# Performance work log

Measured on AMD Instinct MI355X. Metric: run time of the kernel, lower is better.

Reference implementation:

```python
import jax, jax.numpy as jnp
import numpy as np

N = 100000   # nodes
E = 600000   # edges (before self loops)
D = 128      # dim_latent = H*F
H = 4        # heads
F = 32       # out_feats per head
L = 3        # num GATConv layers (conv_0 + 2)


def setup_inputs() -> dict:
    key = jax.random.key(0)
    ks = jax.random.split(key, 10)
    return {
        "weights": jax.random.normal(ks[0], (N,), jnp.float32),
        "lin_W": jax.random.normal(ks[1], (D, 1), jnp.float32) * 0.1,
        "lin_b": jnp.zeros((D,), jnp.float32),
        "fc_W": jax.random.normal(ks[2], (L, D, D), jnp.float32) * (1.0 / np.sqrt(D)),
        "attn_l": jax.random.normal(ks[3], (L, H, F), jnp.float32) * 0.1,
        "attn_r": jax.random.normal(ks[4], (L, H, F), jnp.float32) * 0.1,
        "conv_b": jnp.zeros((L, D), jnp.float32),
        "pred_W": jax.random.normal(ks[5], (1, D), jnp.float32) * 0.1,
        "pred_b": jnp.zeros((1,), jnp.float32),
        "src": jax.random.randint(ks[6], (E,), 0, N, jnp.int32),
        "dst": jax.random.randint(ks[7], (E,), 0, N, jnp.int32),
    }


def _leaky(x, slope):
    return jnp.where(x >= 0, x, slope * x)


def _gat_conv(x, fc_W, attn_l, attn_r, bias, src, dst):
    # DGL GATConv: bias-free fc, per-head additive attention, edge softmax over dst
    h = (x @ fc_W.T).reshape(N, H, F)                      # [N,H,F]
    el = jnp.sum(h * attn_l[None], axis=-1)                # [N,H]
    er = jnp.sum(h * attn_r[None], axis=-1)                # [N,H]
    e = _leaky(el[src] + er[dst], 0.2)                     # [Etot,H]
    m = jax.ops.segment_max(e, dst, num_segments=N)        # [N,H]
    a = jnp.exp(e - m[dst])                                # [Etot,H]
    s = jax.ops.segment_sum(a, dst, num_segments=N)        # [N,H]
    alpha = a / s[dst]                                     # [Etot,H]
    msg = h[src] * alpha[:, :, None]                       # [Etot,H,F]
    out = jax.ops.segment_sum(msg, dst, num_segments=N)    # [N,H,F]
    out = out + bias.reshape(H, F)[None]
    return out.reshape(N, H * F)


def reference(weights, lin_W, lin_b, fc_W, attn_l, attn_r, conv_b, pred_W, pred_b, src, dst):
    # add self loops (dgl.add_self_loop)
    loop = jnp.arange(N, dtype=src.dtype)
    s_full = jnp.concatenate([src, loop])
    d_full = jnp.concatenate([dst, loop])

    x = weights[:, None] @ lin_W.T + lin_b                 # [N,D]
    for i in range(L):
        if i > 0:
            x = _leaky(x, 0.01)                            # nn.LeakyReLU default
        x = _gat_conv(x, fc_W[i], attn_l[i], attn_r[i], conv_b[i], s_full, d_full)
    logits = x @ pred_W.T + pred_b                         # [N,1]
    return logits
```

## Files before the change

kernel.cpp:

```cpp
#include <hip/hip_runtime.h>
#include <hip/hip_bf16.h>
#include <math.h>


__device__ __forceinline__ float leaky02(float x) {
    return x >= 0.f ? x : 0.2f * x;
}
__device__ __forceinline__ float leaky01(float x) {
    return x >= 0.f ? x : 0.01f * x;
}

__device__ __forceinline__ unsigned short f2bf(float f) {
    unsigned u = __float_as_uint(f);
    unsigned r = u + 0x7FFFu + ((u >> 16) & 1u);
    return (unsigned short)(r >> 16);
}
__device__ __forceinline__ float bf2f(unsigned short s) {
    return __uint_as_float(((unsigned)s) << 16);
}

typedef __attribute__((ext_vector_type(8))) short bf16x8;
typedef __attribute__((ext_vector_type(8))) unsigned short u16x8;
typedef __attribute__((ext_vector_type(4))) float f32x4;

__global__ __launch_bounds__(1024) void prep_kernel(
    int* __restrict__ deg, int N,
    const float* __restrict__ fc_W, const float* __restrict__ attn_l,
    const float* __restrict__ attn_r,
    short* __restrict__ Wh, short* __restrict__ Wl,
    short* __restrict__ Mh, short* __restrict__ Ml,
    const float* __restrict__ lW, const float* __restrict__ lb,
    const float* __restrict__ cb2, const float* __restrict__ pW,
    const float* __restrict__ pb,
    float* __restrict__ c1, float* __restrict__ c2, float* __restrict__ prm)
{
    const int nbi = (N + 1023) >> 10;
    const int b = blockIdx.x;
    const int t = threadIdx.x;

    if (b < nbi) {
        int i = b * 1024 + t;
        if (i < N) deg[i] = 1;
        if (i < 2 * 16384) {
            const float* W = fc_W + 16384;
            int l    = i >> 14;
            int p    = i & 16383;
            int j    = p & 7;
            int lane = (p >> 3) & 63;
            int c    = (p >> 9) & 7;
            int kk   = p >> 12;
            int mr   = lane & 15;
            int quad = lane >> 4;
            int row  = c * 16 + mr;
            int d    = kk * 32 + quad * 8 + j;
            float f = W[(size_t)l * 16384 + row * 128 + d];
            unsigned short hi = f2bf(f);
            Wh[i] = (short)hi;
            Wl[i] = (short)f2bf(f - bf2f(hi));
        }
    } else if (b < nbi + 2) {
        int l = b - nbi;
        const float* W  = fc_W + (size_t)(l + 1) * 16384;
        const float* al = attn_l + (l + 1) * 128;
        const float* ar = attn_r + (l + 1) * 128;
        short* mh = Mh + (size_t)l * 16 * 128;
        short* ml = Ml + (size_t)l * 16 * 128;
        int r = t >> 7;
        int d = t & 127;
        int hh = r & 3;
        const float* av = (r < 4) ? al : ar;
        float s = 0.f;
#pragma unroll
        for (int f = 0; f < 32; ++f)
            s += W[(size_t)(hh * 32 + f) * 128 + d] * av[hh * 32 + f];
        unsigned short hi = f2bf(s);
        mh[r * 128 + d] = (short)hi;
        ml[r * 128 + d] = (short)f2bf(s - bf2f(hi));
        mh[(r + 8) * 128 + d] = 0;
        ml[(r + 8) * 128 + d] = 0;
    } else {
        __shared__ float sh1[128], sh2[128], sh3[128], sh4[128], sh5[128];
        const float* W0 = fc_W;
        const float* al = attn_l;
        const float* ar = attn_r;
        int j = t >> 3, sub = t & 7;
        float s1 = 0.f, s2 = 0.f;
        int d0 = sub * 16;
#pragma unroll
        for (int k = 0; k < 16; ++k) {
            float wv = W0[j * 128 + d0 + k];
            s1 += lW[d0 + k] * wv;
            s2 += lb[d0 + k] * wv;
        }
#pragma unroll
        for (int m = 1; m <= 4; m <<= 1) {
            s1 += __shfl_xor(s1, m, 64);
            s2 += __shfl_xor(s2, m, 64);
        }
        if (sub == 0) {
            c1[j] = s1; c2[j] = s2;
            sh1[j] = s1 * al[j]; sh2[j] = s2 * al[j];
            sh3[j] = s1 * ar[j]; sh4[j] = s2 * ar[j];
            sh5[j] = cb2[j] * pW[j];
        }
        __syncthreads();
        if (t < 4) {
            float p = 0.f, q = 0.f, r = 0.f, s = 0.f;
            for (int f = 0; f < 32; ++f) {
                p += sh1[t * 32 + f]; q += sh2[t * 32 + f];
                r += sh3[t * 32 + f]; s += sh4[t * 32 + f];
            }
            prm[t] = p; prm[4 + t] = q; prm[8 + t] = r; prm[12 + t] = s;
        }
        if (t == 0) {
            float cs = 0.f;
            for (int k = 0; k < 128; ++k) cs += sh5[k];
            prm[16] = cs + pb[0];
        }
    }
}

__global__ __launch_bounds__(256) void deg_count_slot_kernel(
    const int* __restrict__ dst, int* __restrict__ deg,
    int* __restrict__ slot, int E)
{
    int i = blockIdx.x * 256 + threadIdx.x;
    if (i < E) slot[i] = atomicAdd(&deg[dst[i]], 1);
}

#define SCAN_TILE 1024

__global__ __launch_bounds__(256) void scanA_kernel(
    const int* __restrict__ deg, int* __restrict__ bsum, int N)
{
    __shared__ int ws[4];
    int b = blockIdx.x, t = threadIdx.x;
    int base = b * SCAN_TILE + t * 4;
    int s = 0;
#pragma unroll
    for (int k = 0; k < 4; ++k) {
        int i = base + k;
        if (i < N) s += deg[i];
    }
#pragma unroll
    for (int m = 32; m >= 1; m >>= 1) s += __shfl_xor(s, m, 64);
    if ((t & 63) == 0) ws[t >> 6] = s;
    __syncthreads();
    if (t == 0) bsum[b] = ws[0] + ws[1] + ws[2] + ws[3];
}

__global__ __launch_bounds__(1024) void scanB_kernel(
    int* __restrict__ bsum, int* __restrict__ bpre, int* __restrict__ rowp,
    int NB, int N)
{
    __shared__ int sh[1024];
    int t = threadIdx.x;
    int v = (t < NB) ? bsum[t] : 0;
    sh[t] = v;
    __syncthreads();
    for (int off = 1; off < 1024; off <<= 1) {
        int u = (t >= off) ? sh[t - off] : 0;
        __syncthreads();
        sh[t] += u;
        __syncthreads();
    }
    if (t < NB) bpre[t] = sh[t] - v;
    if (t == 1023) rowp[N] = sh[1023];
}

__global__ __launch_bounds__(256) void scanC_kernel(
    const int* __restrict__ deg, const int* __restrict__ bpre,
    int* __restrict__ rowp, int* __restrict__ col, int N)
{
    __shared__ int sh[256];
    int b = blockIdx.x, t = threadIdx.x;
    int base = b * SCAN_TILE + t * 4;
    int v[4];
#pragma unroll
    for (int k = 0; k < 4; ++k) {
        int i = base + k;
        v[k] = (i < N) ? deg[i] : 0;
    }
    int tsum = v[0] + v[1] + v[2] + v[3];
    sh[t] = tsum;
    __syncthreads();
    for (int off = 1; off < 256; off <<= 1) {
        int u = (t >= off) ? sh[t - off] : 0;
        __syncthreads();
        sh[t] += u;
        __syncthreads();
    }
    int pre = bpre[b] + sh[t] - tsum;
#pragma unroll
    for (int k = 0; k < 4; ++k) {
        int i = base + k;
        if (i < N) {
            rowp[i] = pre;
            col[pre] = i;
        }
        pre += v[k];
    }
}

__global__ __launch_bounds__(256) void scatter2_kernel(
    const int* __restrict__ src, const int* __restrict__ dst,
    const int* __restrict__ slot, const int* __restrict__ rowp,
    int* __restrict__ col, int E)
{
    int i = blockIdx.x * 256 + threadIdx.x;
    if (i < E) col[rowp[dst[i]] + slot[i]] = src[i];
}

__global__ __launch_bounds__(256) void agg0_kernel(
    const float* __restrict__ w, const float* __restrict__ c1,
    const float* __restrict__ c2, const float* __restrict__ prm,
    const int* __restrict__ rowp, const int* __restrict__ col,
    const float* __restrict__ bias, unsigned short* __restrict__ xout, int N)
{
    const int lane = threadIdx.x & 63;
    const int q    = lane >> 4;
    const int l16  = lane & 15;
    const int v    = blockIdx.x * 16 + (threadIdx.x >> 6) * 4 + q;
    if (v >= N) return;

    const int r0 = rowp[v], r1 = rowp[v + 1];
    const int head = l16 >> 2;
    const int e4   = l16 & 3;
    const int f0   = l16 * 8;
    const float pl = prm[head],     ql = prm[4 + head];
    const float pr = prm[8 + head], qr = prm[12 + head];

    const float wv  = w[v];
    const float erq = wv * pr + qr;
    const float mref = leaky02(wv * pl + ql + erq);

    float S = 0.f, Sw = 0.f;
    for (int j = r0 + e4; j < r1; j += 4) {
        int u = col[j];
        float wu = w[u];
        float e = leaky02(wu * pl + ql + erq);
        float d = fminf(e - mref, 80.f);
        float p = __expf(d);
        S += p; Sw += p * wu;
    }
    S  += __shfl_xor(S, 1, 64);  S  += __shfl_xor(S, 2, 64);
    Sw += __shfl_xor(Sw, 1, 64); Sw += __shfl_xor(Sw, 2, 64);
    const float t = Sw / S;

    float4 a0 = *reinterpret_cast<const float4*>(&c1[f0]);
    float4 a1 = *reinterpret_cast<const float4*>(&c1[f0 + 4]);
    float4 g0 = *reinterpret_cast<const float4*>(&c2[f0]);
    float4 g1 = *reinterpret_cast<const float4*>(&c2[f0 + 4]);
    float4 b0 = *reinterpret_cast<const float4*>(&bias[f0]);
    float4 b1 = *reinterpret_cast<const float4*>(&bias[f0 + 4]);
    const float aa[8] = {a0.x, a0.y, a0.z, a0.w, a1.x, a1.y, a1.z, a1.w};
    const float gg[8] = {g0.x, g0.y, g0.z, g0.w, g1.x, g1.y, g1.z, g1.w};
    const float bb[8] = {b0.x, b0.y, b0.z, b0.w, b1.x, b1.y, b1.z, b1.w};

    u16x8 o;
#pragma unroll
    for (int k = 0; k < 8; ++k)
        o[k] = f2bf(leaky01(t * aa[k] + gg[k] + bb[k]));
    *reinterpret_cast<u16x8*>(&xout[(size_t)v * 128 + f0]) = o;
}

__global__ __launch_bounds__(256) void gemm_mfma_kernel(
    const unsigned short* __restrict__ xb, const short* __restrict__ Wh,
    const short* __restrict__ Wl, const short* __restrict__ Mh,
    const short* __restrict__ Ml, unsigned short* __restrict__ hb,
    float* __restrict__ el, float* __restrict__ er,
    const float* __restrict__ pW, float* __restrict__ yel,
    int N, int mode)
{
    const int lane = threadIdx.x & 63;
    const int wv   = threadIdx.x >> 6;
    const int m0   = blockIdx.x * 128 + wv * 32;
    const int mr   = lane & 15;
    const int quad = lane >> 4;

    int r0 = m0 + mr;      if (r0 > N - 1) r0 = N - 1;
    int r1 = m0 + 16 + mr; if (r1 > N - 1) r1 = N - 1;
    const unsigned short* xp0 = xb + (size_t)r0 * 128 + quad * 8;
    const unsigned short* xp1 = xb + (size_t)r1 * 128 + quad * 8;

    f32x4 acc0[8], acc1[8], acce0, acce1;
#pragma unroll
    for (int c = 0; c < 8; ++c) {
        acc0[c] = (f32x4){0.f, 0.f, 0.f, 0.f};
        acc1[c] = (f32x4){0.f, 0.f, 0.f, 0.f};
    }
    acce0 = (f32x4){0.f, 0.f, 0.f, 0.f};
    acce1 = (f32x4){0.f, 0.f, 0.f, 0.f};

#pragma unroll
    for (int kk = 0; kk < 4; ++kk) {
        bf16x8 a0 = *reinterpret_cast<const bf16x8*>(xp0 + kk * 32);
        bf16x8 a1 = *reinterpret_cast<const bf16x8*>(xp1 + kk * 32);

        const int kb = kk * 32 + quad * 8;
        bf16x8 bh[8], bl[8];
#pragma unroll
        for (int c = 0; c < 8; ++c) {
            const size_t wo = (size_t)((kk * 8 + c) * 64 + lane) * 8;
            bh[c] = *reinterpret_cast<const bf16x8*>(Wh + wo);
            bl[c] = *reinterpret_cast<const bf16x8*>(Wl + wo);
        }
        bf16x8 eh = *reinterpret_cast<const bf16x8*>(Mh + (size_t)mr * 128 + kb);
        bf16x8 eo = *reinterpret_cast<const bf16x8*>(Ml + (size_t)mr * 128 + kb);
#pragma unroll
        for (int c = 0; c < 8; ++c) {
            acc0[c] = __builtin_amdgcn_mfma_f32_16x16x32_bf16(a0, bh[c], acc0[c], 0, 0, 0);
            acc0[c] = __builtin_amdgcn_mfma_f32_16x16x32_bf16(a0, bl[c], acc0[c], 0, 0, 0);
            acc1[c] = __builtin_amdgcn_mfma_f32_16x16x32_bf16(a1, bh[c], acc1[c], 0, 0, 0);
            acc1[c] = __builtin_amdgcn_mfma_f32_16x16x32_bf16(a1, bl[c], acc1[c], 0, 0, 0);
        }
        acce0 = __builtin_amdgcn_mfma_f32_16x16x32_bf16(a0, eh, acce0, 0, 0, 0);
        acce0 = __builtin_amdgcn_mfma_f32_16x16x32_bf16(a0, eo, acce0, 0, 0, 0);
        acce1 = __builtin_amdgcn_mfma_f32_16x16x32_bf16(a1, eh, acce1, 0, 0, 0);
        acce1 = __builtin_amdgcn_mfma_f32_16x16x32_bf16(a1, eo, acce1, 0, 0, 0);
    }

    if (mode == 0) {
#pragma unroll
        for (int i = 0; i < 4; ++i) {
            int rowA = m0 + quad * 4 + i;
            if (rowA < N) {
                unsigned short* hp = hb + (size_t)rowA * 128 + mr;
#pragma unroll
                for (int c = 0; c < 8; ++c) hp[c * 16] = f2bf(acc0[c][i]);
                if (mr < 4)       el[(size_t)rowA * 4 + mr]       = acce0[i];
                else if (mr < 8)  er[(size_t)rowA * 4 + (mr - 4)] = acce0[i];
            }
            int rowB = m0 + 16 + quad * 4 + i;
            if (rowB < N) {
                unsigned short* hp = hb + (size_t)rowB * 128 + mr;
#pragma unroll
                for (int c = 0; c < 8; ++c) hp[c * 16] = f2bf(acc1[c][i]);
                if (mr < 4)       el[(size_t)rowB * 4 + mr]       = acce1[i];
                else if (mr < 8)  er[(size_t)rowB * 4 + (mr - 4)] = acce1[i];
            }
        }
    } else {
        float pw[8];
#pragma unroll
        for (int c = 0; c < 8; ++c) pw[c] = pW[mr + c * 16];
#pragma unroll
        for (int i = 0; i < 4; ++i) {
            int rowA = m0 + quad * 4 + i;
            {
                float y[4];
#pragma unroll
                for (int h = 0; h < 4; ++h)
                    y[h] = acc0[2 * h][i] * pw[2 * h] + acc0[2 * h + 1][i] * pw[2 * h + 1];
#pragma unroll
                for (int d = 1; d < 16; d <<= 1) {
#pragma unroll
                    for (int h = 0; h < 4; ++h) y[h] += __shfl_xor(y[h], d, 64);
                }
                if (rowA < N) {
                    if (mr < 4) {
                        float2 o; o.x = y[mr]; o.y = acce0[i];
                        *reinterpret_cast<float2*>(&yel[(size_t)rowA * 8 + mr * 2]) = o;
                    } else if (mr < 8) {
                        er[(size_t)rowA * 4 + (mr - 4)] = acce0[i];
                    }
                }
            }
            int rowB = m0 + 16 + quad * 4 + i;
            {
                float y[4];
#pragma unroll
                for (int h = 0; h < 4; ++h)
                    y[h] = acc1[2 * h][i] * pw[2 * h] + acc1[2 * h + 1][i] * pw[2 * h + 1];
#pragma unroll
                for (int d = 1; d < 16; d <<= 1) {
#pragma unroll
                    for (int h = 0; h < 4; ++h) y[h] += __shfl_xor(y[h], d, 64);
                }
                if (rowB < N) {
                    if (mr < 4) {
                        float2 o; o.x = y[mr]; o.y = acce1[i];
                        *reinterpret_cast<float2*>(&yel[(size_t)rowB * 8 + mr * 2]) = o;
                    } else if (mr < 8) {
                        er[(size_t)rowB * 4 + (mr - 4)] = acce1[i];
                    }
                }
            }
        }
    }
}

__global__ __launch_bounds__(256) void agg_mid_kernel(
    const unsigned short* __restrict__ hb, const float* __restrict__ el,
    const float* __restrict__ er, const int* __restrict__ rowp,
    const int* __restrict__ col, const float* __restrict__ bias,
    unsigned short* __restrict__ xout, int N)
{
    const int lane = threadIdx.x & 63;
    const int q    = lane >> 4;
    const int l16  = lane & 15;
    const int v    = blockIdx.x * 16 + (threadIdx.x >> 6) * 4 + q;
    if (v >= N) return;

    const int r0 = rowp[v], r1 = rowp[v + 1];
    const int head = l16 >> 2;
    const int f0   = l16 * 8;
    const float erq = er[(size_t)v * 4 + head];
    const float el_self = el[(size_t)v * 4 + head];
    const float mref = leaky02(el_self + erq);

    float s = 0.f;
    float acc[8];
#pragma unroll
    for (int k = 0; k < 8; ++k) acc[k] = 0.f;

    float elA = el_self;
    u16x8 hvA = *reinterpret_cast<const u16x8*>(&hb[(size_t)v * 128 + f0]);
    int jB = (r0 + 1 < r1) ? r0 + 1 : r1 - 1;
    int uB = col[jB];
    float elB = el[(size_t)uB * 4 + head];
    u16x8 hvB = *reinterpret_cast<const u16x8*>(&hb[(size_t)uB * 128 + f0]);

    for (int j = r0; j < r1; j += 2) {
        int jA2 = (j + 2 < r1) ? j + 2 : r1 - 1;
        int uA2 = col[jA2];
        float elA2 = el[(size_t)uA2 * 4 + head];
        u16x8 hvA2 = *reinterpret_cast<const u16x8*>(&hb[(size_t)uA2 * 128 + f0]);

        {
            float e = leaky02(elA + erq);
            float d = fminf(e - mref, 80.f);
            float p = __expf(d);
            s += p;
#pragma unroll
            for (int k = 0; k < 8; ++k) acc[k] += p * bf2f(hvA[k]);
        }

        if (j + 1 < r1) {
            int jB2 = (j + 3 < r1) ? j + 3 : r1 - 1;
            int uB2 = col[jB2];
            float elB2 = el[(size_t)uB2 * 4 + head];
            u16x8 hvB2 = *reinterpret_cast<const u16x8*>(&hb[(size_t)uB2 * 128 + f0]);

            float e = leaky02(elB + erq);
            float d = fminf(e - mref, 80.f);
            float p = __expf(d);
            s += p;
#pragma unroll
            for (int k = 0; k < 8; ++k) acc[k] += p * bf2f(hvB[k]);

            elB = elB2; hvB = hvB2;
        }
        elA = elA2; hvA = hvA2;
    }
    const float is = 1.f / s;

    float4 b0 = *reinterpret_cast<const float4*>(&bias[f0]);
    float4 b1 = *reinterpret_cast<const float4*>(&bias[f0 + 4]);
    const float bb[8] = {b0.x, b0.y, b0.z, b0.w, b1.x, b1.y, b1.z, b1.w};

    u16x8 o;
#pragma unroll
    for (int k = 0; k < 8; ++k) o[k] = f2bf(leaky01(acc[k] * is + bb[k]));
    *reinterpret_cast<u16x8*>(&xout[(size_t)v * 128 + f0]) = o;
}

__global__ __launch_bounds__(256) void agg2_kernel(
    const float* __restrict__ yel, const float* __restrict__ er,
    const int* __restrict__ rowp, const int* __restrict__ col,
    const float* __restrict__ prm, float* __restrict__ logits, int N)
{
    const int lane = threadIdx.x & 63;
    const int q    = lane >> 4;
    const int l16  = lane & 15;
    const int v    = blockIdx.x * 16 + (threadIdx.x >> 6) * 4 + q;
    if (v >= N) return;

    const int r0 = rowp[v], r1 = rowp[v + 1];
    const int head = l16 >> 2;
    const int e4   = l16 & 3;
    const float erq = er[(size_t)v * 4 + head];

    float2 selfy = *reinterpret_cast<const float2*>(&yel[(size_t)v * 8 + head * 2]);
    const float mref = leaky02(selfy.y + erq);

    float S = 0.f, A = 0.f;
    for (int j = r0 + e4; j < r1; j += 4) {
        int u = col[j];
        float2 c = *reinterpret_cast<const float2*>(&yel[(size_t)u * 8 + head * 2]);
        float e = leaky02(c.y + erq);
        float d = fminf(e - mref, 80.f);
        float p = __expf(d);
        S += p; A += p * c.x;
    }
    S += __shfl_xor(S, 1, 64); S += __shfl_xor(S, 2, 64);
    A += __shfl_xor(A, 1, 64); A += __shfl_xor(A, 2, 64);
    float part = A / S;
    part += __shfl_xor(part, 4, 64);
    part += __shfl_xor(part, 8, 64);
    if (l16 == 0) logits[v] = part + prm[16];
}

extern "C" void kernel_launch(void* const* d_in, const int* in_sizes, int n_in,
                              void* d_out, int out_size, void* d_ws, size_t ws_size,
                              hipStream_t stream)
{
    const float* weights = (const float*)d_in[0];
    const float* lin_W   = (const float*)d_in[1];
    const float* lin_b   = (const float*)d_in[2];
    const float* fc_W    = (const float*)d_in[3];
    const float* attn_l  = (const float*)d_in[4];
    const float* attn_r  = (const float*)d_in[5];
    const float* conv_b  = (const float*)d_in[6];
    const float* pred_W  = (const float*)d_in[7];
    const float* pred_b  = (const float*)d_in[8];
    const int*   src     = (const int*)d_in[9];
    const int*   dst     = (const int*)d_in[10];

    const int N = in_sizes[0];
    const int E = in_sizes[9];
    const int NB = (N + SCAN_TILE - 1) / SCAN_TILE;
    const int NBI = (N + 1023) / 1024;

    unsigned short* xb = (unsigned short*)d_ws;
    unsigned short* hb = xb + (size_t)N * 128;
    float* el  = (float*)(hb + (size_t)N * 128);
    float* er  = el + (size_t)N * 4;
    float* yel = er + (size_t)N * 4;
    float* c1  = yel + (size_t)N * 8;
    float* c2  = c1 + 128;
    float* prm = c2 + 128;
    short* Whs = (short*)(prm + 32);
    short* Wls = Whs + 2 * 16384;
    short* Mhs = Wls + 2 * 16384;
    short* Mls = Mhs + 2 * 2048;
    int*   deg  = (int*)(Mls + 2 * 2048);
    int*   rowp = deg + N;
    int*   slot = rowp + (N + 1);
    int*   col  = slot + E;
    int*   bsum = col + (E + N);
    int*   bpre = bsum + NB;

    prep_kernel<<<NBI + 3, 1024, 0, stream>>>(
        deg, N, fc_W, attn_l, attn_r, Whs, Wls, Mhs, Mls,
        lin_W, lin_b, conv_b + 2 * 128, pred_W, pred_b, c1, c2, prm);

    deg_count_slot_kernel<<<(E + 255) / 256, 256, 0, stream>>>(dst, deg, slot, E);
    scanA_kernel<<<NB, 256, 0, stream>>>(deg, bsum, N);
    scanB_kernel<<<1, 1024, 0, stream>>>(bsum, bpre, rowp, NB, N);
    scanC_kernel<<<NB, 256, 0, stream>>>(deg, bpre, rowp, col, N);
    scatter2_kernel<<<(E + 255) / 256, 256, 0, stream>>>(src, dst, slot, rowp, col, E);

    agg0_kernel<<<(N + 15) / 16, 256, 0, stream>>>(
        weights, c1, c2, prm, rowp, col, conv_b, xb, N);

    gemm_mfma_kernel<<<(N + 127) / 128, 256, 0, stream>>>(
        xb, Whs, Wls, Mhs, Mls, hb, el, er, pred_W, yel, N, 0);
    agg_mid_kernel<<<(N + 15) / 16, 256, 0, stream>>>(
        hb, el, er, rowp, col, conv_b + 128, xb, N);

    gemm_mfma_kernel<<<(N + 127) / 128, 256, 0, stream>>>(
        xb, Whs + 16384, Wls + 16384, Mhs + 2048, Mls + 2048,
        hb, el, er, pred_W, yel, N, 1);
    agg2_kernel<<<(N + 15) / 16, 256, 0, stream>>>(
        yel, er, rowp, col, prm, (float*)d_out, N);
}
```

Baseline: 251.8 us.

## Replace three-pass prefix scan with single-pass atomic-base block scan

Merges the three scan kernels into one kernel. Each 1024-node block scans its degrees locally and claims a global base offset through an atomicAdd on a counter zeroed in prep_kernel. Because blocks claim bases in arbitrary order, rows are no longer globally ordered, so the aggregation kernels now compute row ends as rowp[v]+deg[v] instead of reading rowp[v+1]. This removes two kernel launches and their serial dependencies, at the cost of an extra deg read per node and a non-monotonic CSR layout.

```diff
diff --git a/kernel.cpp b/kernel.cpp
--- a/kernel.cpp
+++ b/kernel.cpp
@@ -32,11 +32,13 @@
     const float* __restrict__ lW, const float* __restrict__ lb,
     const float* __restrict__ cb2, const float* __restrict__ pW,
     const float* __restrict__ pb,
-    float* __restrict__ c1, float* __restrict__ c2, float* __restrict__ prm)
+    float* __restrict__ c1, float* __restrict__ c2, float* __restrict__ prm,
+    int* __restrict__ base_ctr)
 {
     const int nbi = (N + 1023) >> 10;
     const int b = blockIdx.x;
     const int t = threadIdx.x;
+    if (b == 0 && t == 0) *base_ctr = 0;
 
     if (b < nbi) {
         int i = b * 1024 + t;
@@ -128,34 +130,15 @@
     if (i < E) slot[i] = atomicAdd(&deg[dst[i]], 1);
 }
 
-#define SCAN_TILE 1024
-
-__global__ __launch_bounds__(256) void scanA_kernel(
-    const int* __restrict__ deg, int* __restrict__ bsum, int N)
-{
-    __shared__ int ws[4];
+__global__ __launch_bounds__(1024) void scan_kernel(
+    const int* __restrict__ deg, int* __restrict__ base_ctr,
+    int* __restrict__ rowp, int* __restrict__ col, int N)
+{
+    __shared__ int sh[1024];
+    __shared__ int sbase;
     int b = blockIdx.x, t = threadIdx.x;
-    int base = b * SCAN_TILE + t * 4;
-    int s = 0;
-#pragma unroll
-    for (int k = 0; k < 4; ++k) {
-        int i = base + k;
-        if (i < N) s += deg[i];
-    }
-#pragma unroll
-    for (int m = 32; m >= 1; m >>= 1) s += __shfl_xor(s, m, 64);
-    if ((t & 63) == 0) ws[t >> 6] = s;
-    __syncthreads();
-    if (t == 0) bsum[b] = ws[0] + ws[1] + ws[2] + ws[3];
-}
-
-__global__ __launch_bounds__(1024) void scanB_kernel(
-    int* __restrict__ bsum, int* __restrict__ bpre, int* __restrict__ rowp,
-    int NB, int N)
-{
-    __shared__ int sh[1024];
-    int t = threadIdx.x;
-    int v = (t < NB) ? bsum[t] : 0;
+    int i = b * 1024 + t;
+    int v = (i < N) ? deg[i] : 0;
     sh[t] = v;
     __syncthreads();
     for (int off = 1; off < 1024; off <<= 1) {
@@ -164,41 +147,12 @@
         sh[t] += u;
         __syncthreads();
     }
-    if (t < NB) bpre[t] = sh[t] - v;
-    if (t == 1023) rowp[N] = sh[1023];
-}
-
-__global__ __launch_bounds__(256) void scanC_kernel(
-    const int* __restrict__ deg, const int* __restrict__ bpre,
-    int* __restrict__ rowp, int* __restrict__ col, int N)
-{
-    __shared__ int sh[256];
-    int b = blockIdx.x, t = threadIdx.x;
-    int base = b * SCAN_TILE + t * 4;
-    int v[4];
-#pragma unroll
-    for (int k = 0; k < 4; ++k) {
-        int i = base + k;
-        v[k] = (i < N) ? deg[i] : 0;
-    }
-    int tsum = v[0] + v[1] + v[2] + v[3];
-    sh[t] = tsum;
+    if (t == 1023) sbase = atomicAdd(base_ctr, sh[1023]);
     __syncthreads();
-    for (int off = 1; off < 256; off <<= 1) {
-        int u = (t >= off) ? sh[t - off] : 0;
-        __syncthreads();
-        sh[t] += u;
-        __syncthreads();
-    }
-    int pre = bpre[b] + sh[t] - tsum;
-#pragma unroll
-    for (int k = 0; k < 4; ++k) {
-        int i = base + k;
-        if (i < N) {
-            rowp[i] = pre;
-            col[pre] = i;
-        }
-        pre += v[k];
+    int pre = sbase + sh[t] - v;
+    if (i < N) {
+        rowp[i] = pre;
+        col[pre] = i;
     }
 }
 
@@ -214,8 +168,9 @@
 __global__ __launch_bounds__(256) void agg0_kernel(
     const float* __restrict__ w, const float* __restrict__ c1,
     const float* __restrict__ c2, const float* __restrict__ prm,
-    const int* __restrict__ rowp, const int* __restrict__ col,
-    const float* __restrict__ bias, unsigned short* __restrict__ xout, int N)
+    const int* __restrict__ rowp, const int* __restrict__ deg,
+    const int* __restrict__ col, const float* __restrict__ bias,
+    unsigned short* __restrict__ xout, int N)
 {
     const int lane = threadIdx.x & 63;
     const int q    = lane >> 4;
@@ -223,7 +178,8 @@
     const int v    = blockIdx.x * 16 + (threadIdx.x >> 6) * 4 + q;
     if (v >= N) return;
 
-    const int r0 = rowp[v], r1 = rowp[v + 1];
+    const int r0 = rowp[v];
+    const int r1 = r0 + deg[v];
     const int head = l16 >> 2;
     const int e4   = l16 & 3;
     const int f0   = l16 * 8;
@@ -393,8 +349,8 @@
 __global__ __launch_bounds__(256) void agg_mid_kernel(
     const unsigned short* __restrict__ hb, const float* __restrict__ el,
     const float* __restrict__ er, const int* __restrict__ rowp,
-    const int* __restrict__ col, const float* __restrict__ bias,
-    unsigned short* __restrict__ xout, int N)
+    const int* __restrict__ deg, const int* __restrict__ col,
+    const float* __restrict__ bias, unsigned short* __restrict__ xout, int N)
 {
     const int lane = threadIdx.x & 63;
     const int q    = lane >> 4;
@@ -402,7 +358,8 @@
     const int v    = blockIdx.x * 16 + (threadIdx.x >> 6) * 4 + q;
     if (v >= N) return;
 
-    const int r0 = rowp[v], r1 = rowp[v + 1];
+    const int r0 = rowp[v];
+    const int r1 = r0 + deg[v];
     const int head = l16 >> 2;
     const int f0   = l16 * 8;
     const float erq = er[(size_t)v * 4 + head];
@@ -467,8 +424,9 @@
 
 __global__ __launch_bounds__(256) void agg2_kernel(
     const float* __restrict__ yel, const float* __restrict__ er,
-    const int* __restrict__ rowp, const int* __restrict__ col,
-    const float* __restrict__ prm, float* __restrict__ logits, int N)
+    const int* __restrict__ rowp, const int* __restrict__ deg,
+    const int* __restrict__ col, const float* __restrict__ prm,
+    float* __restrict__ logits, int N)
 {
     const int lane = threadIdx.x & 63;
     const int q    = lane >> 4;
@@ -476,7 +434,8 @@
     const int v    = blockIdx.x * 16 + (threadIdx.x >> 6) * 4 + q;
     if (v >= N) return;
 
-    const int r0 = rowp[v], r1 = rowp[v + 1];
+    const int r0 = rowp[v];
+    const int r1 = r0 + deg[v];
     const int head = l16 >> 2;
     const int e4   = l16 & 3;
     const float erq = er[(size_t)v * 4 + head];
@@ -519,8 +478,7 @@
 
     const int N = in_sizes[0];
     const int E = in_sizes[9];
-    const int NB = (N + SCAN_TILE - 1) / SCAN_TILE;
-    const int NBI = (N + 1023) / 1024;
+    const int NB1024 = (N + 1023) / 1024;
 
     unsigned short* xb = (unsigned short*)d_ws;
     unsigned short* hb = xb + (size_t)N * 128;
@@ -538,30 +496,31 @@
     int*   rowp = deg + N;
     int*   slot = rowp + (N + 1);
     int*   col  = slot + E;
-    int*   bsum = col + (E + N);
-    int*   bpre = bsum + NB;
-
-    prep_kernel<<<NBI + 3, 1024, 0, stream>>>(
+    int*   bctr = col + (E + N);
+
+    prep_kernel<<<NB1024 + 3, 1024, 0, stream>>>(
         deg, N, fc_W, attn_l, attn_r, Whs, Wls, Mhs, Mls,
-        lin_W, lin_b, conv_b + 2 * 128, pred_W, pred_b, c1, c2, prm);
+        lin_W, lin_b, conv_b + 2 * 128, pred_W, pred_b, c1, c2, prm, bctr);
 
     deg_count_slot_kernel<<<(E + 255) / 256, 256, 0, stream>>>(dst, deg, slot, E);
-    scanA_kernel<<<NB, 256, 0, stream>>>(deg, bsum, N);
-    scanB_kernel<<<1, 1024, 0, stream>>>(bsum, bpre, rowp, NB, N);
-    scanC_kernel<<<NB, 256, 0, stream>>>(deg, bpre, rowp, col, N);
+
+    scan_kernel<<<NB1024, 1024, 0, stream>>>(deg, bctr, rowp, col, N);
+
     scatter2_kernel<<<(E + 255) / 256, 256, 0, stream>>>(src, dst, slot, rowp, col, E);
 
     agg0_kernel<<<(N + 15) / 16, 256, 0, stream>>>(
-        weights, c1, c2, prm, rowp, col, conv_b, xb, N);
+        weights, c1, c2, prm, rowp, deg, col, conv_b, xb, N);
 
     gemm_mfma_kernel<<<(N + 127) / 128, 256, 0, stream>>>(
         xb, Whs, Wls, Mhs, Mls, hb, el, er, pred_W, yel, N, 0);
+
     agg_mid_kernel<<<(N + 15) / 16, 256, 0, stream>>>(
-        hb, el, er, rowp, col, conv_b + 128, xb, N);
+        hb, el, er, rowp, deg, col, conv_b + 128, xb, N);
 
     gemm_mfma_kernel<<<(N + 127) / 128, 256, 0, stream>>>(
         xb, Whs + 16384, Wls + 16384, Mhs + 2048, Mls + 2048,
         hb, el, er, pred_W, yel, N, 1);
+
     agg2_kernel<<<(N + 15) / 16, 256, 0, stream>>>(
-        yel, er, rowp, col, prm, (float*)d_out, N);
-}
+        yel, er, rowp, deg, col, prm, (float*)d_out, N);
+}
```

After: 248.5 us, median of 2. Within noise of the previous version (-1.3%).
